# Kernel tuning notes

Hardware: AMD Instinct MI355X
Metric: run time of the kernel (lower is better)

Reference implementation:

```python
import jax, jax.numpy as jnp
import numpy as np

B = 2048
D = 40960          # util.half_kp_numel(): 64 king squares * 640 piece-square planes
BASE = 288
MOVE = 4096        # util.move_numel(): 64 from-squares * 64 to-squares
MOVE_SIZE = (64, 64)


def setup_inputs() -> dict:
    key = jax.random.key(0)
    ks = jax.random.split(key, 24)
    f32 = jnp.float32
    # forward args: sparse one-hot half-kp occupancy vectors (modeled as rand floats)
    pov = (jax.random.uniform(ks[0], (B, 1), f32) > 0.5).astype(f32)
    white = (jax.random.uniform(ks[1], (B, D), f32) < 0.001).astype(f32)
    black = (jax.random.uniform(ks[2], (B, D), f32) < 0.001).astype(f32)
    s = 0.01
    p = {
        'W_w': jax.random.normal(ks[3], (BASE, D), f32) * s,
        'b_w': jnp.zeros((BASE,), f32),
        'W_b': jax.random.normal(ks[4], (BASE, D), f32) * s,
        'b_b': jnp.zeros((BASE,), f32),
        'W_v0': jax.random.normal(ks[5], (32, 2 * BASE), f32) * s,
        'b_v0': jnp.zeros((32,), f32),
        'W_v1': jax.random.normal(ks[6], (32, 32), f32) * s,
        'b_v1': jnp.zeros((32,), f32),
        'W_v2': jax.random.normal(ks[7], (1, 32), f32) * s,
        'b_v2': jnp.zeros((1,), f32),
        'W_a0': jax.random.normal(ks[8], (144, 2 * BASE), f32) * s,
        'b_a0': jnp.zeros((144,), f32),
        'W_a1': jax.random.normal(ks[9], (MOVE, 144), f32) * s,
        'b_a1': jnp.zeros((MOVE,), f32),
        'W_vs': jax.random.normal(ks[10], (1, 2 * BASE), f32) * s,
        'b_vs': jnp.zeros((1,), f32),
        'W_as': jax.random.normal(ks[11], (MOVE, 2 * BASE), f32) * s,
        'b_as': jnp.zeros((MOVE,), f32),
    }
    return dict(pov=pov, white=white, black=black, **p)


def _linear(x, W, b):
    return x @ W.T + b


def reference(pov, white, black, W_w, b_w, W_b, b_b,
              W_v0, b_v0, W_v1, b_v1, W_v2, b_v2,
              W_a0, b_a0, W_a1, b_a1, W_vs, b_vs, W_as, b_as):
    # half-kp affine accumulators (the sparse gather-sum candidate)
    w256 = _linear(white, W_w, b_w)            # [B, BASE]
    b256 = _linear(black, W_b, b_b)            # [B, BASE]
    cat_wb = jnp.concatenate([w256, b256], axis=1)
    cat_bw = jnp.concatenate([b256, w256], axis=1)
    base = jax.nn.relu(pov * cat_wb + (1.0 - pov) * cat_bw)  # [B, 2*BASE]
    # value head with skip
    val = jax.nn.relu(_linear(base, W_v0, b_v0))
    val = jax.nn.relu(_linear(val, W_v1, b_v1))
    val = _linear(val, W_v2, b_v2) + _linear(base, W_vs, b_vs)   # [B, 1]
    # action head with skip
    act = jax.nn.relu(_linear(base, W_a0, b_a0))
    act = _linear(act, W_a1, b_a1) + _linear(base, W_as, b_as)   # [B, MOVE]
    act = act.reshape(act.shape[0], *MOVE_SIZE)                  # [B, 64, 64]
    return (val, act)
```

## Files before the change

kernel.cpp:

```cpp
#include <hip/hip_runtime.h>

#define D_IN 40960
#define NB 2048
#define BASEN 288
#define CAPL 95
#define KP 736

typedef __attribute__((ext_vector_type(4))) float f32x4;
typedef __attribute__((ext_vector_type(8))) short short8;

__device__ inline float bf2f(ushort u) {
    unsigned v = ((unsigned)u) << 16; float f; __builtin_memcpy(&f, &v, 4); return f;
}
__device__ inline ushort f2bf(float f) {
    unsigned x; __builtin_memcpy(&x, &f, 4);
    unsigned r = (x + 0x7FFFu + ((x >> 16) & 1u)) >> 16; return (ushort)r;
}

__device__ inline void llds16(const void* g, void* l) {
    __builtin_amdgcn_global_load_lds((const __attribute__((address_space(1))) unsigned*)g,
                                     (__attribute__((address_space(3))) unsigned*)l, 16, 0, 0);
}

__global__ __launch_bounds__(256) void transpose_kernel(const float* __restrict__ Ww,
                                                        const float* __restrict__ Wb,
                                                        ushort* __restrict__ Wtw,
                                                        ushort* __restrict__ Wtb) {
    const float* src = blockIdx.y ? Wb : Ww;
    ushort* dst = blockIdx.y ? Wtb : Wtw;
    __shared__ float lt[32][292];
    int t = threadIdx.x;
    int d0 = blockIdx.x * 32;
    int orr = t >> 3, dc = (t & 7) * 4;
#pragma unroll
    for (int p = 0; p < 9; ++p) {
        int o = p * 32 + orr;
        float4 u = *(const float4*)&src[(size_t)o * D_IN + d0 + dc];
        lt[dc][o] = u.x; lt[dc + 1][o] = u.y; lt[dc + 2][o] = u.z; lt[dc + 3][o] = u.w;
    }
    __syncthreads();
    ushort* db = dst + (size_t)d0 * BASEN;
#pragma unroll
    for (int p = 0; p < 5; ++p) {
        int s = p * 256 + t;
        if (s < 1152) {
            int d = s / 36, m = s - d * 36;
            const float* lp = &lt[d][m * 8];
            short8 v;
            v[0] = (short)f2bf(lp[0]); v[1] = (short)f2bf(lp[1]);
            v[2] = (short)f2bf(lp[2]); v[3] = (short)f2bf(lp[3]);
            v[4] = (short)f2bf(lp[4]); v[5] = (short)f2bf(lp[5]);
            v[6] = (short)f2bf(lp[6]); v[7] = (short)f2bf(lp[7]);
            *(short8*)&db[s * 8] = v;
        }
    }
}

__global__ __launch_bounds__(256) void prep_kernel(const float* __restrict__ W_a1,
                                                   const float* __restrict__ W_as,
                                                   const float* __restrict__ b_a1,
                                                   const float* __restrict__ b_as,
                                                   const float* __restrict__ W_a0,
                                                   const float* __restrict__ W_v0,
                                                   ushort* __restrict__ Wcat,
                                                   float* __restrict__ biasA,
                                                   ushort* __restrict__ Wa0h,
                                                   ushort* __restrict__ Wv0h) {
    int m = blockIdx.x, t = threadIdx.x;
    if (m < 4096) {
        ushort* dst = Wcat + (size_t)m * KP;
        if (t < 144) dst[t] = f2bf(W_a1[(size_t)m * 144 + t]);
        if (t >= 144 && t < 160) dst[t] = 0;
        for (int j = t; j < 576; j += 256) dst[160 + j] = f2bf(W_as[(size_t)m * 576 + j]);
        if (t == 200) biasA[m] = b_a1[m] + b_as[m];
    } else if (m < 4096 + 144) {
        int r = m - 4096;
        for (int j = t; j < 576; j += 256) Wa0h[(size_t)r * 576 + j] = f2bf(W_a0[(size_t)r * 576 + j]);
    } else {
        int r = m - (4096 + 144);
        for (int j = t; j < 576; j += 256) Wv0h[(size_t)r * 576 + j] = f2bf(W_v0[(size_t)r * 576 + j]);
    }
}

__global__ __launch_bounds__(256) void scan_kernel(const float* __restrict__ white,
                                                   const float* __restrict__ black,
                                                   const ushort* __restrict__ Wtw,
                                                   const ushort* __restrict__ Wtb,
                                                   const float* __restrict__ b_w,
                                                   const float* __restrict__ b_b,
                                                   float* __restrict__ accG) {
    const int row = blockIdx.x;
    const int colr = blockIdx.y;
    const int t = threadIdx.x;
    __shared__ int cnt;
    __shared__ int idx[CAPL];
    if (t == 0) cnt = 0;
    __syncthreads();

    const uint4* src = (const uint4*)((colr ? black : white) + (size_t)row * D_IN);
#pragma unroll
    for (int b16 = 0; b16 < 2; ++b16) {
        uint4 x[16];
#pragma unroll
        for (int u = 0; u < 16; ++u) x[u] = src[b16 * 4096 + u * 256 + t];
#pragma unroll
        for (int u = 0; u < 16; ++u) {
            uint4 v = x[u];
            if (v.x | v.y | v.z | v.w) {
                int i4 = (b16 * 4096 + u * 256 + t) * 4;
                if (v.x) { int p = atomicAdd(&cnt, 1); if (p < CAPL) idx[p] = i4; }
                if (v.y) { int p = atomicAdd(&cnt, 1); if (p < CAPL) idx[p] = i4 + 1; }
                if (v.z) { int p = atomicAdd(&cnt, 1); if (p < CAPL) idx[p] = i4 + 2; }
                if (v.w) { int p = atomicAdd(&cnt, 1); if (p < CAPL) idx[p] = i4 + 3; }
            }
        }
    }
    {
        uint4 x[8];
#pragma unroll
        for (int u = 0; u < 8; ++u) x[u] = src[8192 + u * 256 + t];
#pragma unroll
        for (int u = 0; u < 8; ++u) {
            uint4 v = x[u];
            if (v.x | v.y | v.z | v.w) {
                int i4 = (8192 + u * 256 + t) * 4;
                if (v.x) { int p = atomicAdd(&cnt, 1); if (p < CAPL) idx[p] = i4; }
                if (v.y) { int p = atomicAdd(&cnt, 1); if (p < CAPL) idx[p] = i4 + 1; }
                if (v.z) { int p = atomicAdd(&cnt, 1); if (p < CAPL) idx[p] = i4 + 2; }
                if (v.w) { int p = atomicAdd(&cnt, 1); if (p < CAPL) idx[p] = i4 + 3; }
            }
        }
    }
    __syncthreads();

    if (t < 144) {
        const ushort* Wt = colr ? Wtb : Wtw;
        const float* bb = colr ? b_b : b_w;
        int n = min(cnt, CAPL);
        float a0 = bb[2 * t], a1 = bb[2 * t + 1];
#pragma unroll 4
        for (int i = 0; i < n; ++i) {
            unsigned q = *(const unsigned*)&Wt[(size_t)idx[i] * BASEN + 2 * t];
            a0 += bf2f((ushort)(q & 0xFFFF));
            a1 += bf2f((ushort)(q >> 16));
        }
        float2 r; r.x = a0; r.y = a1;
        *(float2*)&accG[((size_t)colr * NB + row) * BASEN + 2 * t] = r;
    }
}

__global__ __launch_bounds__(576) void head_kernel(const float* __restrict__ accG,
                                                   const float* __restrict__ pov,
                                                   const ushort* __restrict__ Wa0h,
                                                   const float* __restrict__ b_a0,
                                                   const ushort* __restrict__ Wv0h,
                                                   const float* __restrict__ b_v0,
                                                   const float* __restrict__ W_v1,
                                                   const float* __restrict__ b_v1,
                                                   const float* __restrict__ W_v2,
                                                   const float* __restrict__ b_v2,
                                                   const float* __restrict__ W_vs,
                                                   const float* __restrict__ b_vs,
                                                   ushort* __restrict__ hidden,
                                                   float* __restrict__ outv) {
    int b = blockIdx.x, t = threadIdx.x;
    __shared__ float baseS[576];
    __shared__ float v0s[32];
    __shared__ float skipS;

    float p = pov[b];
    ushort* hrow = hidden + (size_t)b * KP;
    if (t < BASEN) {
        float aW = accG[(size_t)b * BASEN + t];
        float aB = accG[(size_t)NB * BASEN + (size_t)b * BASEN + t];
        float b0 = fmaxf(p * aW + (1.0f - p) * aB, 0.0f);
        float b1 = fmaxf(p * aB + (1.0f - p) * aW, 0.0f);
        baseS[t] = b0; baseS[BASEN + t] = b1;
        hrow[160 + t] = f2bf(b0);
        hrow[160 + BASEN + t] = f2bf(b1);
        if (t < 16) hrow[144 + t] = 0;
    }
    __syncthreads();

    {
        int o = t >> 2, q4 = t & 3;
        const ushort* wr = Wa0h + (size_t)o * 576 + q4 * 144;
        const float* bp = &baseS[q4 * 144];
        float s = 0.f;
#pragma unroll
        for (int j = 0; j < 144; j += 8) {
            uint4 q = *(const uint4*)(wr + j);
            s += bp[j + 0] * bf2f((ushort)(q.x & 0xFFFF)) + bp[j + 1] * bf2f((ushort)(q.x >> 16))
               + bp[j + 2] * bf2f((ushort)(q.y & 0xFFFF)) + bp[j + 3] * bf2f((ushort)(q.y >> 16))
               + bp[j + 4] * bf2f((ushort)(q.z & 0xFFFF)) + bp[j + 5] * bf2f((ushort)(q.z >> 16))
               + bp[j + 6] * bf2f((ushort)(q.w & 0xFFFF)) + bp[j + 7] * bf2f((ushort)(q.w >> 16));
        }
        s += __shfl_xor(s, 1);
        s += __shfl_xor(s, 2);
        if (q4 == 0) hrow[o] = f2bf(fmaxf(s + b_a0[o], 0.f));
    }

    if (t < 512) {
        int o = t >> 4, sub = t & 15;
        const ushort* wr = Wv0h + (size_t)o * 576 + sub * 36;
        const float* bp = &baseS[sub * 36];
        float s = 0.f;
#pragma unroll
        for (int j = 0; j < 36; j += 4) {
            ushort4 q = *(const ushort4*)(wr + j);
            s += bp[j + 0] * bf2f(q.x) + bp[j + 1] * bf2f(q.y)
               + bp[j + 2] * bf2f(q.z) + bp[j + 3] * bf2f(q.w);
        }
        s += __shfl_xor(s, 1); s += __shfl_xor(s, 2);
        s += __shfl_xor(s, 4); s += __shfl_xor(s, 8);
        if (sub == 0) v0s[o] = fmaxf(s + b_v0[o], 0.f);
    } else {
        int u = t - 512;
        const float* wp = W_vs + u * 9;
        const float* bp = &baseS[u * 9];
        float s = 0.f;
#pragma unroll
        for (int j = 0; j < 9; ++j) s += bp[j] * wp[j];
        s += __shfl_xor(s, 1); s += __shfl_xor(s, 2); s += __shfl_xor(s, 4);
        s += __shfl_xor(s, 8); s += __shfl_xor(s, 16); s += __shfl_xor(s, 32);
        if (u == 0) skipS = s;
    }
    __syncthreads();

    if (t < 32) {
        float s = b_v1[t];
        const float* w = W_v1 + (size_t)t * 32;
#pragma unroll
        for (int j = 0; j < 32; ++j) s += v0s[j] * w[j];
        float part = fmaxf(s, 0.f) * W_v2[t];
        part += __shfl_xor(part, 1); part += __shfl_xor(part, 2); part += __shfl_xor(part, 4);
        part += __shfl_xor(part, 8); part += __shfl_xor(part, 16);
        if (t == 0) outv[b] = part + b_v2[0] + skipS + b_vs[0];
    }
}

__global__ __launch_bounds__(256) void gemm_act(const ushort* __restrict__ A,
                                                const ushort* __restrict__ Bm,
                                                const float* __restrict__ biasA,
                                                float* __restrict__ outa) {
    __shared__ ushort As[128 * 32];
    __shared__ ushort Bs[128 * 32];
    int tid = threadIdx.x;
    int lane = tid & 63, wv = tid >> 6;
    int bm = blockIdx.x, bn = blockIdx.y;
    int wm = wv & 1, wn = wv >> 1;
    f32x4 acc[4][4];
#pragma unroll
    for (int mt = 0; mt < 4; ++mt)
#pragma unroll
        for (int nt = 0; nt < 4; ++nt) { f32x4 z = {0.f, 0.f, 0.f, 0.f}; acc[mt][nt] = z; }

    int r = tid >> 2, c8 = (tid & 3) * 8;
    const ushort* Ag = A  + (size_t)(bm * 128 + r) * KP + c8;
    const ushort* Bg = Bm + (size_t)(bn * 128 + r) * KP + c8;
    ushort* AsW = As + wv * 512;
    ushort* BsW = Bs + wv * 512;

    int kg = (lane >> 4) * 8;
    int rA = wm * 64 + (lane & 15);
    int rB = wn * 64 + (lane & 15);

    for (int kk = 0; kk < KP; kk += 32) {
        llds16(Ag + kk, AsW);
        llds16(Ag + (size_t)64 * KP + kk, AsW + 2048);
        llds16(Bg + kk, BsW);
        llds16(Bg + (size_t)64 * KP + kk, BsW + 2048);
        __syncthreads();
        short8 af[4], bf[4];
#pragma unroll
        for (int mt = 0; mt < 4; ++mt) af[mt] = *(const short8*)&As[(rA + mt * 16) * 32 + kg];
#pragma unroll
        for (int nt = 0; nt < 4; ++nt) bf[nt] = *(const short8*)&Bs[(rB + nt * 16) * 32 + kg];
#pragma unroll
        for (int mt = 0; mt < 4; ++mt)
#pragma unroll
            for (int nt = 0; nt < 4; ++nt)
                acc[mt][nt] = __builtin_amdgcn_mfma_f32_16x16x32_bf16(af[mt], bf[nt], acc[mt][nt], 0, 0, 0);
        __syncthreads();
    }

    int colb = bn * 128 + wn * 64 + (lane & 15);
    int rowb = bm * 128 + wm * 64 + ((lane >> 4) << 2);
#pragma unroll
    for (int nt = 0; nt < 4; ++nt) {
        float bia = biasA[colb + nt * 16];
#pragma unroll
        for (int mt = 0; mt < 4; ++mt) {
#pragma unroll
            for (int q = 0; q < 4; ++q) {
                int rr = rowb + mt * 16 + q;
                outa[(size_t)rr * 4096 + colb + nt * 16] = acc[mt][nt][q] + bia;
            }
        }
    }
}

extern "C" void kernel_launch(void* const* d_in, const int* in_sizes, int n_in,
                              void* d_out, int out_size, void* d_ws, size_t ws_size,
                              hipStream_t stream) {
    const float* pov   = (const float*)d_in[0];
    const float* white = (const float*)d_in[1];
    const float* black = (const float*)d_in[2];
    const float* W_w   = (const float*)d_in[3];
    const float* b_w   = (const float*)d_in[4];
    const float* W_b   = (const float*)d_in[5];
    const float* b_b   = (const float*)d_in[6];
    const float* W_v0  = (const float*)d_in[7];
    const float* b_v0  = (const float*)d_in[8];
    const float* W_v1  = (const float*)d_in[9];
    const float* b_v1  = (const float*)d_in[10];
    const float* W_v2  = (const float*)d_in[11];
    const float* b_v2  = (const float*)d_in[12];
    const float* W_a0  = (const float*)d_in[13];
    const float* b_a0  = (const float*)d_in[14];
    const float* W_a1  = (const float*)d_in[15];
    const float* b_a1  = (const float*)d_in[16];
    const float* W_vs  = (const float*)d_in[17];
    const float* b_vs  = (const float*)d_in[18];
    const float* W_as  = (const float*)d_in[19];
    const float* b_as  = (const float*)d_in[20];

    char* ws = (char*)d_ws;
    ushort* Wtw   = (ushort*)(ws + 0);
    ushort* Wtb   = (ushort*)(ws + 23592960);
    ushort* hidden= (ushort*)(ws + 47185920);
    ushort* Wcat  = (ushort*)(ws + 50200576);
    float*  biasA = (float*)(ws + 56229888);
    ushort* Wa0h  = (ushort*)(ws + 56246272);
    ushort* Wv0h  = (ushort*)(ws + 56412160);
    float*  accG  = (float*)(ws + 56449024);

    float* outp = (float*)d_out;

    transpose_kernel<<<dim3(D_IN / 32, 2), 256, 0, stream>>>(W_w, W_b, Wtw, Wtb);
    prep_kernel<<<4096 + 144 + 32, 256, 0, stream>>>(W_a1, W_as, b_a1, b_as, W_a0, W_v0,
                                                     Wcat, biasA, Wa0h, Wv0h);
    scan_kernel<<<dim3(NB, 2), 256, 0, stream>>>(white, black, Wtw, Wtb, b_w, b_b, accG);
    head_kernel<<<NB, 576, 0, stream>>>(accG, pov, Wa0h, b_a0, Wv0h, b_v0,
                                        W_v1, b_v1, W_v2, b_v2, W_vs, b_vs, hidden, outp);
    gemm_act<<<dim3(2048 / 128, 4096 / 128), 256, 0, stream>>>(hidden, Wcat, biasA, outp + 2048);
}
```

Baseline: 841.0 us.

## Merge input scan with weight prep into one kernel using ballot bitmasks

```diff
diff --git a/kernel.cpp b/kernel.cpp
--- a/kernel.cpp
+++ b/kernel.cpp
@@ -5,6 +5,7 @@
 #define BASEN 288
 #define CAPL 95
 #define KP 736
+#define MASKW 160
 
 typedef __attribute__((ext_vector_type(4))) float f32x4;
 typedef __attribute__((ext_vector_type(8))) short short8;
@@ -22,114 +23,130 @@
                                      (__attribute__((address_space(3))) unsigned*)l, 16, 0, 0);
 }
 
-__global__ __launch_bounds__(256) void transpose_kernel(const float* __restrict__ Ww,
-                                                        const float* __restrict__ Wb,
-                                                        ushort* __restrict__ Wtw,
-                                                        ushort* __restrict__ Wtb) {
-    const float* src = blockIdx.y ? Wb : Ww;
-    ushort* dst = blockIdx.y ? Wtb : Wtw;
-    __shared__ float lt[32][292];
-    int t = threadIdx.x;
-    int d0 = blockIdx.x * 32;
-    int orr = t >> 3, dc = (t & 7) * 4;
-#pragma unroll
-    for (int p = 0; p < 9; ++p) {
-        int o = p * 32 + orr;
-        float4 u = *(const float4*)&src[(size_t)o * D_IN + d0 + dc];
-        lt[dc][o] = u.x; lt[dc + 1][o] = u.y; lt[dc + 2][o] = u.z; lt[dc + 3][o] = u.w;
-    }
-    __syncthreads();
-    ushort* db = dst + (size_t)d0 * BASEN;
-#pragma unroll
-    for (int p = 0; p < 5; ++p) {
-        int s = p * 256 + t;
-        if (s < 1152) {
-            int d = s / 36, m = s - d * 36;
-            const float* lp = &lt[d][m * 8];
-            short8 v;
-            v[0] = (short)f2bf(lp[0]); v[1] = (short)f2bf(lp[1]);
-            v[2] = (short)f2bf(lp[2]); v[3] = (short)f2bf(lp[3]);
-            v[4] = (short)f2bf(lp[4]); v[5] = (short)f2bf(lp[5]);
-            v[6] = (short)f2bf(lp[6]); v[7] = (short)f2bf(lp[7]);
-            *(short8*)&db[s * 8] = v;
-        }
-    }
-}
-
-__global__ __launch_bounds__(256) void prep_kernel(const float* __restrict__ W_a1,
+__global__ __launch_bounds__(256) void mega_kernel(const float* __restrict__ white,
+                                                   const float* __restrict__ black,
+                                                   const float* __restrict__ Ww,
+                                                   const float* __restrict__ Wb,
+                                                   const float* __restrict__ W_a1,
                                                    const float* __restrict__ W_as,
                                                    const float* __restrict__ b_a1,
                                                    const float* __restrict__ b_as,
                                                    const float* __restrict__ W_a0,
                                                    const float* __restrict__ W_v0,
+                                                   ushort* __restrict__ Wtw,
+                                                   ushort* __restrict__ Wtb,
+                                                   unsigned long long* __restrict__ maskArr,
                                                    ushort* __restrict__ Wcat,
                                                    float* __restrict__ biasA,
                                                    ushort* __restrict__ Wa0h,
                                                    ushort* __restrict__ Wv0h) {
-    int m = blockIdx.x, t = threadIdx.x;
-    if (m < 4096) {
-        ushort* dst = Wcat + (size_t)m * KP;
-        if (t < 144) dst[t] = f2bf(W_a1[(size_t)m * 144 + t]);
-        if (t >= 144 && t < 160) dst[t] = 0;
-        for (int j = t; j < 576; j += 256) dst[160 + j] = f2bf(W_as[(size_t)m * 576 + j]);
-        if (t == 200) biasA[m] = b_a1[m] + b_as[m];
-    } else if (m < 4096 + 144) {
-        int r = m - 4096;
-        for (int j = t; j < 576; j += 256) Wa0h[(size_t)r * 576 + j] = f2bf(W_a0[(size_t)r * 576 + j]);
+    __shared__ float lt[32][292];
+    int bid = blockIdx.x, t = threadIdx.x;
+
+    if (bid < 4096) {
+        int colr = bid >> 11, row = bid & 2047;
+        const uint4* src = (const uint4*)((colr ? black : white) + (size_t)row * D_IN);
+        unsigned long long* mrow = maskArr + (size_t)bid * MASKW;
+        int wv = t >> 6;
+#pragma unroll
+        for (int g = 0; g < 5; ++g) {
+            uint4 x[8];
+#pragma unroll
+            for (int u = 0; u < 8; ++u) x[u] = src[g * 2048 + u * 256 + t];
+#pragma unroll
+            for (int u = 0; u < 8; ++u) {
+                uint4 v = x[u];
+                unsigned long long m = __ballot((v.x | v.y | v.z | v.w) != 0);
+                if ((t & 63) == 0) mrow[g * 32 + u * 4 + wv] = m;
+            }
+        }
+    } else if (bid < 4096 + 2560) {
+        int tb = bid - 4096;
+        int colr = tb >= 1280;
+        const float* src = colr ? Wb : Ww;
+        ushort* dst = colr ? Wtb : Wtw;
+        int d0 = (tb - colr * 1280) * 32;
+        int orr = t >> 3, dc = (t & 7) * 4;
+#pragma unroll
+        for (int p = 0; p < 9; ++p) {
+            int o = p * 32 + orr;
+            float4 u = *(const float4*)&src[(size_t)o * D_IN + d0 + dc];
+            lt[dc][o] = u.x; lt[dc + 1][o] = u.y; lt[dc + 2][o] = u.z; lt[dc + 3][o] = u.w;
+        }
+        __syncthreads();
+        ushort* db = dst + (size_t)d0 * BASEN;
+#pragma unroll
+        for (int p = 0; p < 5; ++p) {
+            int s = p * 256 + t;
+            if (s < 1152) {
+                int d = s / 36, m = s - d * 36;
+                const float* lp = &lt[d][m * 8];
+                short8 v;
+                v[0] = (short)f2bf(lp[0]); v[1] = (short)f2bf(lp[1]);
+                v[2] = (short)f2bf(lp[2]); v[3] = (short)f2bf(lp[3]);
+                v[4] = (short)f2bf(lp[4]); v[5] = (short)f2bf(lp[5]);
+                v[6] = (short)f2bf(lp[6]); v[7] = (short)f2bf(lp[7]);
+                *(short8*)&db[s * 8] = v;
+            }
+        }
     } else {
-        int r = m - (4096 + 144);
-        for (int j = t; j < 576; j += 256) Wv0h[(size_t)r * 576 + j] = f2bf(W_v0[(size_t)r * 576 + j]);
-    }
-}
-
-__global__ __launch_bounds__(256) void scan_kernel(const float* __restrict__ white,
-                                                   const float* __restrict__ black,
-                                                   const ushort* __restrict__ Wtw,
-                                                   const ushort* __restrict__ Wtb,
-                                                   const float* __restrict__ b_w,
-                                                   const float* __restrict__ b_b,
-                                                   float* __restrict__ accG) {
+        int m = bid - (4096 + 2560);
+        if (m < 4096) {
+            ushort* dst = Wcat + (size_t)m * KP;
+            if (t < 144) dst[t] = f2bf(W_a1[(size_t)m * 144 + t]);
+            if (t >= 144 && t < 160) dst[t] = 0;
+            for (int j = t; j < 576; j += 256) dst[160 + j] = f2bf(W_as[(size_t)m * 576 + j]);
+            if (t == 200) biasA[m] = b_a1[m] + b_as[m];
+        } else if (m < 4096 + 144) {
+            int r = m - 4096;
+            for (int j = t; j < 576; j += 256) Wa0h[(size_t)r * 576 + j] = f2bf(W_a0[(size_t)r * 576 + j]);
+        } else {
+            int r = m - (4096 + 144);
+            for (int j = t; j < 576; j += 256) Wv0h[(size_t)r * 576 + j] = f2bf(W_v0[(size_t)r * 576 + j]);
+        }
+    }
+}
+
+__global__ __launch_bounds__(256) void gather_kernel(const float* __restrict__ white,
+                                                     const float* __restrict__ black,
+                                                     const unsigned long long* __restrict__ maskArr,
+                                                     const ushort* __restrict__ Wtw,
+                                                     const ushort* __restrict__ Wtb,
+                                                     const float* __restrict__ b_w,
+                                                     const float* __restrict__ b_b,
+                                                     float* __restrict__ accG) {
     const int row = blockIdx.x;
     const int colr = blockIdx.y;
     const int t = threadIdx.x;
-    __shared__ int cnt;
+    const int rc = colr * NB + row;
+    __shared__ int pcnt, cnt;
+    __shared__ int probe[CAPL];
     __shared__ int idx[CAPL];
-    if (t == 0) cnt = 0;
+    if (t == 0) pcnt = 0;
+    if (t == 1) cnt = 0;
+    __syncthreads();
+
+    if (t < MASKW) {
+        unsigned long long m = maskArr[(size_t)rc * MASKW + t];
+        while (m) {
+            int b = __ffsll(m) - 1;
+            m &= m - 1;
+            int p = atomicAdd(&pcnt, 1);
+            if (p < CAPL) probe[p] = t * 64 + b;
+        }
+    }
     __syncthreads();
 
     const uint4* src = (const uint4*)((colr ? black : white) + (size_t)row * D_IN);
-#pragma unroll
-    for (int b16 = 0; b16 < 2; ++b16) {
-        uint4 x[16];
-#pragma unroll
-        for (int u = 0; u < 16; ++u) x[u] = src[b16 * 4096 + u * 256 + t];
-#pragma unroll
-        for (int u = 0; u < 16; ++u) {
-            uint4 v = x[u];
-            if (v.x | v.y | v.z | v.w) {
-                int i4 = (b16 * 4096 + u * 256 + t) * 4;
-                if (v.x) { int p = atomicAdd(&cnt, 1); if (p < CAPL) idx[p] = i4; }
-                if (v.y) { int p = atomicAdd(&cnt, 1); if (p < CAPL) idx[p] = i4 + 1; }
-                if (v.z) { int p = atomicAdd(&cnt, 1); if (p < CAPL) idx[p] = i4 + 2; }
-                if (v.w) { int p = atomicAdd(&cnt, 1); if (p < CAPL) idx[p] = i4 + 3; }
-            }
-        }
-    }
-    {
-        uint4 x[8];
-#pragma unroll
-        for (int u = 0; u < 8; ++u) x[u] = src[8192 + u * 256 + t];
-#pragma unroll
-        for (int u = 0; u < 8; ++u) {
-            uint4 v = x[u];
-            if (v.x | v.y | v.z | v.w) {
-                int i4 = (8192 + u * 256 + t) * 4;
-                if (v.x) { int p = atomicAdd(&cnt, 1); if (p < CAPL) idx[p] = i4; }
-                if (v.y) { int p = atomicAdd(&cnt, 1); if (p < CAPL) idx[p] = i4 + 1; }
-                if (v.z) { int p = atomicAdd(&cnt, 1); if (p < CAPL) idx[p] = i4 + 2; }
-                if (v.w) { int p = atomicAdd(&cnt, 1); if (p < CAPL) idx[p] = i4 + 3; }
-            }
-        }
+    int np = min(pcnt, CAPL);
+    for (int p = t; p < np; p += 256) {
+        int pi = probe[p];
+        uint4 v = src[pi];
+        int i4 = pi * 4;
+        if (v.x) { int q = atomicAdd(&cnt, 1); if (q < CAPL) idx[q] = i4; }
+        if (v.y) { int q = atomicAdd(&cnt, 1); if (q < CAPL) idx[q] = i4 + 1; }
+        if (v.z) { int q = atomicAdd(&cnt, 1); if (q < CAPL) idx[q] = i4 + 2; }
+        if (v.w) { int q = atomicAdd(&cnt, 1); if (q < CAPL) idx[q] = i4 + 3; }
     }
     __syncthreads();
 
@@ -334,13 +351,14 @@
     ushort* Wa0h  = (ushort*)(ws + 56246272);
     ushort* Wv0h  = (ushort*)(ws + 56412160);
     float*  accG  = (float*)(ws + 56449024);
+    unsigned long long* maskArr = (unsigned long long*)(ws + 61167616);
 
     float* outp = (float*)d_out;
 
-    transpose_kernel<<<dim3(D_IN / 32, 2), 256, 0, stream>>>(W_w, W_b, Wtw, Wtb);
-    prep_kernel<<<4096 + 144 + 32, 256, 0, stream>>>(W_a1, W_as, b_a1, b_as, W_a0, W_v0,
-                                                     Wcat, biasA, Wa0h, Wv0h);
-    scan_kernel<<<dim3(NB, 2), 256, 0, stream>>>(white, black, Wtw, Wtb, b_w, b_b, accG);
+    mega_kernel<<<4096 + 2560 + 4272, 256, 0, stream>>>(white, black, W_w, W_b,
+                                                        W_a1, W_as, b_a1, b_as, W_a0, W_v0,
+                                                        Wtw, Wtb, maskArr, Wcat, biasA, Wa0h, Wv0h);
+    gather_kernel<<<dim3(NB, 2), 256, 0, stream>>>(white, black, maskArr, Wtw, Wtb, b_w, b_b, accG);
     head_kernel<<<NB, 576, 0, stream>>>(accG, pov, Wa0h, b_a0, Wv0h, b_v0,
                                         W_v1, b_v1, W_v2, b_v2, W_vs, b_vs, hidden, outp);
     gemm_act<<<dim3(2048 / 128, 4096 / 128), 256, 0, stream>>>(hidden, Wcat, biasA, outp + 2048);
```

New measurement: 839.2 us. No clear change (-0.2%).
